# Optimization experiments

Measured on AMD Instinct MI355X. Metric: run time of the kernel, lower is better.

The kernel has to match this reference:

```python
import jax, jax.numpy as jnp
import numpy as np
import math

INPUTDIM = 256
OUTDIM = 512
GRIDSIZE = 64

def setup_inputs() -> dict:
    key = jax.random.key(0)
    k1, k2 = jax.random.split(key)
    x = jax.random.normal(k1, (4096, INPUTDIM), dtype=jnp.float32)
    # init: randn / (sqrt(inputdim) * sqrt(gridsize))  (smooth_initialization=False)
    fouriercoeffs = jax.random.normal(k2, (2, OUTDIM, INPUTDIM, GRIDSIZE), dtype=jnp.float32) / (
        math.sqrt(INPUTDIM) * math.sqrt(GRIDSIZE))
    bias = jnp.zeros((1, OUTDIM), dtype=jnp.float32)
    return {"x": x, "fouriercoeffs": fouriercoeffs, "bias": bias}

def reference(x, fouriercoeffs, bias):
    # x: [N, I]; fouriercoeffs: [2, O, I, G]; bias: [1, O]
    k = jnp.arange(1, GRIDSIZE + 1, dtype=x.dtype)          # [G]
    kx = x[:, :, None] * k[None, None, :]                   # [N, I, G]
    c = jnp.cos(kx)
    s = jnp.sin(kx)
    # contraction over (I, G) — GEMM-equivalent of the naive broadcast-sum
    y = jnp.einsum('nig,oig->no', c, fouriercoeffs[0])
    y = y + jnp.einsum('nig,oig->no', s, fouriercoeffs[1])
    y = y + bias
    return y
```

## Files before the change

kernel.cpp:

```cpp
#include <hip/hip_runtime.h>
#include <hip/hip_bf16.h>

#define IDIM 256
#define GDIM 64
#define ODIM 512
#define KD   (IDIM * GDIM)
#define TILE_SHORTS (512 * 64)
#define WS_NEED ((size_t)512 * TILE_SHORTS * 2)

typedef __attribute__((ext_vector_type(8))) short bhalf8;
typedef __attribute__((ext_vector_type(4))) float fvec4;
typedef __attribute__((ext_vector_type(4))) unsigned uvec4;

#define INV2PI 0.15915494309189535f
#define AS1 __attribute__((address_space(1)))
#define AS3 __attribute__((address_space(3)))

static __device__ __forceinline__ short bf16b(float v) {
    __hip_bfloat16 hb = __float2bfloat16(v);
    short s; __builtin_memcpy(&s, &hb, 2); return s;
}
static __device__ __forceinline__ unsigned cvtpk(float lo, float hi) {
    unsigned r;
    asm("v_cvt_pk_bf16_f32 %0, %1, %2" : "=v"(r) : "v"(lo), "v"(hi));
    return r;
}

#define ADVP(A,B,C2) do { float _t = __builtin_fmaf((C2),(B),-(A)); (A)=(B); (B)=_t; \
                          _t = __builtin_fmaf((C2),(B),-(A)); (A)=(B); (B)=_t; } while (0)

__global__ void prep_b(const float* __restrict__ coeffs, short* __restrict__ ws) {
    const int b = blockIdx.x;
    const int i = b >> 1, h = b & 1;
    const int o = threadIdx.x;
    short* dst = ws + ((size_t)b * 512 + o) * 64;
    const int swz = (o & 7) << 4;
#pragma unroll
    for (int j = 0; j < 8; ++j) {
        const int z = j >> 2, Qq = j & 3;
        const float* src = coeffs + ((size_t)z * ODIM + o) * KD
                         + (size_t)i * GDIM + 16 * Qq + 8 * h;
        fvec4 v0 = ((const fvec4*)src)[0];
        fvec4 v1 = ((const fvec4*)src)[1];
        bhalf8 pk;
#pragma unroll
        for (int u = 0; u < 4; ++u) { pk[u] = bf16b(v0[u]); pk[4 + u] = bf16b(v1[u]); }
        *(bhalf8*)((char*)dst + ((j * 16) ^ swz)) = pk;
    }
}

__global__ void bias_init(const float* __restrict__ bias, float* __restrict__ out) {
    int idx = blockIdx.x * 256 + threadIdx.x;
    fvec4 bv = ((const fvec4*)bias)[idx & 127];
    ((fvec4*)out)[idx] = bv;
}

#define FENCE() do { asm volatile("s_waitcnt vmcnt(0) lgkmcnt(0)" ::: "memory"); \
                     __builtin_amdgcn_sched_barrier(0); \
                     __syncthreads(); } while (0)

template<int USE_WS>
__global__ void __launch_bounds__(256, 4)
fkan_gemm(const float* __restrict__ x, const float* __restrict__ coeffs,
          const short* __restrict__ wsb, float* __restrict__ out) {
    __shared__ __align__(16) short B_lds[2][128 * 64];
    __shared__ float  sl_rev[4][128];
    __shared__ float2 sl_cs[4][128];

    const int bx = blockIdx.x;
    const int xcd = bx & 7, j = bx >> 3;
    const int lg  = xcd * 4 + (j & 3);
    const int mt  = j >> 2;
    const int ot  = lg >> 3, ks = lg & 7;
    const int row0 = mt * 128, col0 = ot * 128;
    const int i0 = ks * 32;

    const int t = threadIdx.x;
    const int lane = t & 63, wid = t >> 6;
    const int kl  = (lane >> 4) * 16;
    const int msk = (lane & 7) << 4;
    const int rA0 = wid * 32 + (lane & 15);
    const float m0f = (float)(16 * (lane >> 4) + 1);

    fvec4 acc[2][8];
#pragma unroll
    for (int a = 0; a < 2; ++a)
#pragma unroll
        for (int b = 0; b < 8; ++b) acc[a][b] = (fvec4)0.0f;

    auto fill_sl = [&](int chunk) {
#pragma unroll
        for (int w2 = 0; w2 < 2; ++w2) {
            int idx = lane + w2 * 64;
            int il2 = idx & 3, r2 = wid * 32 + (idx >> 2);
            float xv = x[(size_t)(row0 + r2) * IDIM + i0 + chunk * 4 + il2];
            float rev = xv * INV2PI;
            float a = __builtin_amdgcn_fractf(rev);
            float2 cs;
            cs.x = __builtin_amdgcn_cosf(a);
            cs.y = __builtin_amdgcn_sinf(a);
            sl_rev[il2][r2] = rev;
            sl_cs[il2][r2] = cs;
        }
    };

    auto dmaB = [&](int T1) {
        const short* src = wsb + (size_t)(i0 * 2 + T1) * TILE_SHORTS
                         + (size_t)col0 * 64 + (size_t)t * 8;
        const int bsel = T1 & 1;
#pragma unroll
        for (int q = 0; q < 4; ++q)
            __builtin_amdgcn_global_load_lds(
                (const AS1 unsigned*)(src + q * 2048),
                (AS3 unsigned*)&B_lds[bsel][q * 2048 + wid * 512],
                16, 0, 0);
    };

    auto stage_fb = [&](int T1) {
        const int bsel = T1 & 1;
        const int i = i0 + (T1 >> 1), hh = T1 & 1;
        const int o = t >> 1, z = t & 1;
        char* drow = (char*)&B_lds[bsel][o * 64];
        const int swz = (o & 7) << 4;
#pragma unroll
        for (int Qq = 0; Qq < 4; ++Qq) {
            const float* src = coeffs + ((size_t)z * ODIM + col0 + o) * KD
                             + (size_t)i * GDIM + 16 * Qq + 8 * hh;
            fvec4 v0 = ((const fvec4*)src)[0];
            fvec4 v1 = ((const fvec4*)src)[1];
            bhalf8 pk;
#pragma unroll
            for (int u = 0; u < 4; ++u) { pk[u] = bf16b(v0[u]); pk[4 + u] = bf16b(v1[u]); }
            *(bhalf8*)(drow + ((z * 64 + Qq * 16) ^ swz)) = pk;
        }
    };

    float ccA0, ccB0, ccA1, ccB1;
    float ssA0, ssB0, ssA1, ssB1;
    float C20, C21;
    bhalf8 afc[2], afs[2];

    auto seed_even = [&](int Te) {
        const int il = (Te >> 1) & 3;
#pragma unroll
        for (int fm = 0; fm < 2; ++fm) {
            const int rr = rA0 + fm * 16;
            float rev = sl_rev[il][rr];
            float2 cs1 = sl_cs[il][rr];
            float C2x = cs1.x + cs1.x;
            float a0 = __builtin_amdgcn_fractf(rev * m0f);
            float c0 = __builtin_amdgcn_cosf(a0);
            float s0 = __builtin_amdgcn_sinf(a0);
            float cBv = __builtin_fmaf(c0, cs1.x, -(s0 * cs1.y));
            float sBv = __builtin_fmaf(s0, cs1.x,  c0 * cs1.y);
            uvec4 u; u[0] = cvtpk(c0, cBv);
            float A = c0, B = cBv;
            ADVP(A, B, C2x); u[1] = cvtpk(A, B);
            ADVP(A, B, C2x); u[2] = cvtpk(A, B);
            ADVP(A, B, C2x); u[3] = cvtpk(A, B);
            if (fm == 0) { ccA0 = A; ccB0 = B; ssA0 = s0; ssB0 = sBv; C20 = C2x; }
            else         { ccA1 = A; ccB1 = B; ssA1 = s0; ssB1 = sBv; C21 = C2x; }
            afc[fm] = __builtin_bit_cast(bhalf8, u);
        }
    };

    auto mfma_z = [&](const char* Bb, int z, bhalf8 a0f, bhalf8 a1f) {
        const int koff = (z * 64 + kl) ^ msk;
#pragma unroll
        for (int half = 0; half < 2; ++half) {
            bhalf8 bq[4];
#pragma unroll
            for (int f4 = 0; f4 < 4; ++f4)
                bq[f4] = *(const bhalf8*)(Bb +
                    (size_t)(half * 64 + f4 * 16 + (lane & 15)) * 128 + koff);
            __builtin_amdgcn_s_setprio(1);
#pragma unroll
            for (int f4 = 0; f4 < 4; ++f4) {
                acc[0][half * 4 + f4] = __builtin_amdgcn_mfma_f32_16x16x32_bf16(
                    a0f, bq[f4], acc[0][half * 4 + f4], 0, 0, 0);
                acc[1][half * 4 + f4] = __builtin_amdgcn_mfma_f32_16x16x32_bf16(
                    a1f, bq[f4], acc[1][half * 4 + f4], 0, 0, 0);
            }
            __builtin_amdgcn_s_setprio(0);
        }
    };

    fill_sl(0);
    asm volatile("s_waitcnt lgkmcnt(0)" ::: "memory");
    __builtin_amdgcn_sched_barrier(0);
    seed_even(0);
    if (USE_WS) { dmaB(0); FENCE(); }
    else        { __syncthreads(); }

#pragma unroll 1
    for (int T = 0; T < 64; ++T) {
        if (USE_WS) {
            if ((T & 7) == 6 && T < 62) fill_sl((T + 2) >> 3);
            if (T < 63) dmaB(T + 1);
            __builtin_amdgcn_sched_barrier(0);
        } else {
            if ((T & 7) == 6 && T < 62) fill_sl((T + 2) >> 3);
            stage_fb(T);
            __syncthreads();
        }

        const char* Bb = (const char*)&B_lds[T & 1][0];

        mfma_z(Bb, 0, afc[0], afc[1]);
        if ((T & 1) == 0) {
#pragma unroll
            for (int fm = 0; fm < 2; ++fm) {
                float A = fm ? ssA1 : ssA0, B = fm ? ssB1 : ssB0;
                float C2x = fm ? C21 : C20;
                uvec4 u; u[0] = cvtpk(A, B);
                ADVP(A, B, C2x); u[1] = cvtpk(A, B);
                ADVP(A, B, C2x); u[2] = cvtpk(A, B);
                ADVP(A, B, C2x); u[3] = cvtpk(A, B);
                if (fm == 0) { ssA0 = A; ssB0 = B; } else { ssA1 = A; ssB1 = B; }
                afs[fm] = __builtin_bit_cast(bhalf8, u);
            }
        } else {
#pragma unroll
            for (int fm = 0; fm < 2; ++fm) {
                float A = fm ? ssA1 : ssA0, B = fm ? ssB1 : ssB0;
                float C2x = fm ? C21 : C20;
                uvec4 u;
                ADVP(A, B, C2x); u[0] = cvtpk(A, B);
                ADVP(A, B, C2x); u[1] = cvtpk(A, B);
                ADVP(A, B, C2x); u[2] = cvtpk(A, B);
                ADVP(A, B, C2x); u[3] = cvtpk(A, B);
                afs[fm] = __builtin_bit_cast(bhalf8, u);
            }
        }

        mfma_z(Bb, 1, afs[0], afs[1]);
        if (T < 63) {
            if ((T & 1) == 0) {
#pragma unroll
                for (int fm = 0; fm < 2; ++fm) {
                    float A = fm ? ccA1 : ccA0, B = fm ? ccB1 : ccB0;
                    float C2x = fm ? C21 : C20;
                    uvec4 u;
                    ADVP(A, B, C2x); u[0] = cvtpk(A, B);
                    ADVP(A, B, C2x); u[1] = cvtpk(A, B);
                    ADVP(A, B, C2x); u[2] = cvtpk(A, B);
                    ADVP(A, B, C2x); u[3] = cvtpk(A, B);
                    afc[fm] = __builtin_bit_cast(bhalf8, u);
                }
            } else {
                seed_even(T + 1);
            }
        }

        if (USE_WS) FENCE(); else __syncthreads();
    }

#pragma unroll
    for (int fm = 0; fm < 2; ++fm) {
#pragma unroll
        for (int f = 0; f < 8; ++f) {
            int col = col0 + f * 16 + (lane & 15);
#pragma unroll
            for (int r = 0; r < 4; ++r) {
                int row = row0 + wid * 32 + fm * 16 + ((lane >> 4) * 4) + r;
                atomicAdd(&out[(size_t)row * ODIM + col], acc[fm][f][r]);
            }
        }
    }
}

extern "C" void kernel_launch(void* const* d_in, const int* in_sizes, int n_in,
                              void* d_out, int out_size, void* d_ws, size_t ws_size,
                              hipStream_t stream) {
    (void)in_sizes; (void)n_in; (void)out_size;
    const float* x      = (const float*)d_in[0];
    const float* coeffs = (const float*)d_in[1];
    const float* bias   = (const float*)d_in[2];
    float* out = (float*)d_out;

    const bool use_ws = (ws_size >= WS_NEED) && (((uintptr_t)d_ws & 15) == 0);

    bias_init<<<dim3(2048), dim3(256), 0, stream>>>(bias, out);
    if (use_ws) {
        prep_b<<<dim3(512), dim3(512), 0, stream>>>(coeffs, (short*)d_ws);
        fkan_gemm<1><<<dim3(1024), dim3(256), 0, stream>>>(x, coeffs, (const short*)d_ws, out);
    } else {
        fkan_gemm<0><<<dim3(1024), dim3(256), 0, stream>>>(x, coeffs, nullptr, out);
    }
}
```

Baseline: 176.1 us.

## Switch wave tiling to 2x2 layout and unroll loop by two steps

The four waves now tile the 128x128 output block as 2x2 quadrants of 64x64 instead of four 32-row strips covering all 128 columns. Each wave loads 4 B fragments per k-step instead of 8, but must generate 4 A fragments of cos/sin instead of 2, so more transcendental and recurrence work is done per wave. The main loop is unrolled by two with fixed LDS buffer indices, and the A-fragment generation is interleaved with the MFMA calls. This trades LDS read traffic for extra VALU work and register pressure.

```diff
diff --git a/kernel.cpp b/kernel.cpp
--- a/kernel.cpp
+++ b/kernel.cpp
@@ -77,22 +77,24 @@
 
     const int t = threadIdx.x;
     const int lane = t & 63, wid = t >> 6;
+    const int wave_m = wid & 1, wave_n = wid >> 1;
     const int kl  = (lane >> 4) * 16;
     const int msk = (lane & 7) << 4;
-    const int rA0 = wid * 32 + (lane & 15);
+    const int rA0 = wave_m * 64 + (lane & 15);
+    const int cB0 = wave_n * 64 + (lane & 15);
     const float m0f = (float)(16 * (lane >> 4) + 1);
 
-    fvec4 acc[2][8];
-#pragma unroll
-    for (int a = 0; a < 2; ++a)
-#pragma unroll
-        for (int b = 0; b < 8; ++b) acc[a][b] = (fvec4)0.0f;
+    fvec4 acc[4][4];
+#pragma unroll
+    for (int a = 0; a < 4; ++a)
+#pragma unroll
+        for (int b = 0; b < 4; ++b) acc[a][b] = (fvec4)0.0f;
 
     auto fill_sl = [&](int chunk) {
 #pragma unroll
         for (int w2 = 0; w2 < 2; ++w2) {
-            int idx = lane + w2 * 64;
-            int il2 = idx & 3, r2 = wid * 32 + (idx >> 2);
+            int idx = t + w2 * 256;
+            int il2 = idx & 3, r2 = idx >> 2;
             float xv = x[(size_t)(row0 + r2) * IDIM + i0 + chunk * 4 + il2];
             float rev = xv * INV2PI;
             float a = __builtin_amdgcn_fractf(rev);
@@ -135,135 +137,160 @@
         }
     };
 
-    float ccA0, ccB0, ccA1, ccB1;
-    float ssA0, ssB0, ssA1, ssB1;
-    float C20, C21;
-    bhalf8 afc[2], afs[2];
-
-    auto seed_even = [&](int Te) {
-        const int il = (Te >> 1) & 3;
-#pragma unroll
-        for (int fm = 0; fm < 2; ++fm) {
-            const int rr = rA0 + fm * 16;
-            float rev = sl_rev[il][rr];
-            float2 cs1 = sl_cs[il][rr];
-            float C2x = cs1.x + cs1.x;
-            float a0 = __builtin_amdgcn_fractf(rev * m0f);
-            float c0 = __builtin_amdgcn_cosf(a0);
-            float s0 = __builtin_amdgcn_sinf(a0);
-            float cBv = __builtin_fmaf(c0, cs1.x, -(s0 * cs1.y));
-            float sBv = __builtin_fmaf(s0, cs1.x,  c0 * cs1.y);
-            uvec4 u; u[0] = cvtpk(c0, cBv);
-            float A = c0, B = cBv;
-            ADVP(A, B, C2x); u[1] = cvtpk(A, B);
-            ADVP(A, B, C2x); u[2] = cvtpk(A, B);
-            ADVP(A, B, C2x); u[3] = cvtpk(A, B);
-            if (fm == 0) { ccA0 = A; ccB0 = B; ssA0 = s0; ssB0 = sBv; C20 = C2x; }
-            else         { ccA1 = A; ccB1 = B; ssA1 = s0; ssB1 = sBv; C21 = C2x; }
-            afc[fm] = __builtin_bit_cast(bhalf8, u);
-        }
-    };
-
-    auto mfma_z = [&](const char* Bb, int z, bhalf8 a0f, bhalf8 a1f) {
-        const int koff = (z * 64 + kl) ^ msk;
-#pragma unroll
-        for (int half = 0; half < 2; ++half) {
-            bhalf8 bq[4];
-#pragma unroll
-            for (int f4 = 0; f4 < 4; ++f4)
-                bq[f4] = *(const bhalf8*)(Bb +
-                    (size_t)(half * 64 + f4 * 16 + (lane & 15)) * 128 + koff);
-            __builtin_amdgcn_s_setprio(1);
-#pragma unroll
-            for (int f4 = 0; f4 < 4; ++f4) {
-                acc[0][half * 4 + f4] = __builtin_amdgcn_mfma_f32_16x16x32_bf16(
-                    a0f, bq[f4], acc[0][half * 4 + f4], 0, 0, 0);
-                acc[1][half * 4 + f4] = __builtin_amdgcn_mfma_f32_16x16x32_bf16(
-                    a1f, bq[f4], acc[1][half * 4 + f4], 0, 0, 0);
-            }
-            __builtin_amdgcn_s_setprio(0);
-        }
-    };
+    float kcA[4], kcB[4], ksA[4], ksB[4], kC2[4];
 
     fill_sl(0);
-    asm volatile("s_waitcnt lgkmcnt(0)" ::: "memory");
-    __builtin_amdgcn_sched_barrier(0);
-    seed_even(0);
     if (USE_WS) { dmaB(0); FENCE(); }
     else        { __syncthreads(); }
 
 #pragma unroll 1
-    for (int T = 0; T < 64; ++T) {
-        if (USE_WS) {
-            if ((T & 7) == 6 && T < 62) fill_sl((T + 2) >> 3);
-            if (T < 63) dmaB(T + 1);
-            __builtin_amdgcn_sched_barrier(0);
-        } else {
-            if ((T & 7) == 6 && T < 62) fill_sl((T + 2) >> 3);
-            stage_fb(T);
-            __syncthreads();
-        }
-
-        const char* Bb = (const char*)&B_lds[T & 1][0];
-
-        mfma_z(Bb, 0, afc[0], afc[1]);
-        if ((T & 1) == 0) {
-#pragma unroll
-            for (int fm = 0; fm < 2; ++fm) {
-                float A = fm ? ssA1 : ssA0, B = fm ? ssB1 : ssB0;
-                float C2x = fm ? C21 : C20;
-                uvec4 u; u[0] = cvtpk(A, B);
-                ADVP(A, B, C2x); u[1] = cvtpk(A, B);
-                ADVP(A, B, C2x); u[2] = cvtpk(A, B);
-                ADVP(A, B, C2x); u[3] = cvtpk(A, B);
-                if (fm == 0) { ssA0 = A; ssB0 = B; } else { ssA1 = A; ssB1 = B; }
-                afs[fm] = __builtin_bit_cast(bhalf8, u);
-            }
-        } else {
-#pragma unroll
-            for (int fm = 0; fm < 2; ++fm) {
-                float A = fm ? ssA1 : ssA0, B = fm ? ssB1 : ssB0;
-                float C2x = fm ? C21 : C20;
-                uvec4 u;
-                ADVP(A, B, C2x); u[0] = cvtpk(A, B);
-                ADVP(A, B, C2x); u[1] = cvtpk(A, B);
-                ADVP(A, B, C2x); u[2] = cvtpk(A, B);
-                ADVP(A, B, C2x); u[3] = cvtpk(A, B);
-                afs[fm] = __builtin_bit_cast(bhalf8, u);
-            }
-        }
-
-        mfma_z(Bb, 1, afs[0], afs[1]);
-        if (T < 63) {
-            if ((T & 1) == 0) {
-#pragma unroll
-                for (int fm = 0; fm < 2; ++fm) {
-                    float A = fm ? ccA1 : ccA0, B = fm ? ccB1 : ccB0;
-                    float C2x = fm ? C21 : C20;
+    for (int ii = 0; ii < 32; ++ii) {
+        const int il = ii & 3;
+
+        {
+            const int T = 2 * ii;
+            if (USE_WS) {
+                dmaB(T + 1);
+                __builtin_amdgcn_sched_barrier(0);
+            } else {
+                stage_fb(T);
+                __syncthreads();
+            }
+            const char* Bb = (const char*)&B_lds[0][0];
+
+            {
+                bhalf8 bq[4];
+#pragma unroll
+                for (int fn = 0; fn < 4; ++fn)
+                    bq[fn] = *(const bhalf8*)(Bb +
+                        (size_t)(cB0 + fn * 16) * 128 + (kl ^ msk));
+#pragma unroll
+                for (int fm = 0; fm < 4; ++fm) {
+                    const int rr = rA0 + fm * 16;
+                    float rev = sl_rev[il][rr];
+                    float2 cs1 = sl_cs[il][rr];
+                    float C2x = cs1.x + cs1.x;
+                    float a0 = __builtin_amdgcn_fractf(rev * m0f);
+                    float c0 = __builtin_amdgcn_cosf(a0);
+                    float s0 = __builtin_amdgcn_sinf(a0);
+                    float cBv = __builtin_fmaf(c0, cs1.x, -(s0 * cs1.y));
+                    float sBv = __builtin_fmaf(s0, cs1.x,  c0 * cs1.y);
+                    uvec4 u; u[0] = cvtpk(c0, cBv);
+                    float A = c0, B = cBv;
+                    ADVP(A, B, C2x); u[1] = cvtpk(A, B);
+                    ADVP(A, B, C2x); u[2] = cvtpk(A, B);
+                    ADVP(A, B, C2x); u[3] = cvtpk(A, B);
+                    kcA[fm] = A; kcB[fm] = B; ksA[fm] = s0; ksB[fm] = sBv; kC2[fm] = C2x;
+                    bhalf8 af = __builtin_bit_cast(bhalf8, u);
+                    __builtin_amdgcn_s_setprio(1);
+#pragma unroll
+                    for (int fn = 0; fn < 4; ++fn)
+                        acc[fm][fn] = __builtin_amdgcn_mfma_f32_16x16x32_bf16(
+                            af, bq[fn], acc[fm][fn], 0, 0, 0);
+                    __builtin_amdgcn_s_setprio(0);
+                }
+            }
+            {
+                bhalf8 bq[4];
+#pragma unroll
+                for (int fn = 0; fn < 4; ++fn)
+                    bq[fn] = *(const bhalf8*)(Bb +
+                        (size_t)(cB0 + fn * 16) * 128 + ((64 + kl) ^ msk));
+#pragma unroll
+                for (int fm = 0; fm < 4; ++fm) {
+                    float C2x = kC2[fm];
+                    float A = ksA[fm], B = ksB[fm];
+                    uvec4 u; u[0] = cvtpk(A, B);
+                    ADVP(A, B, C2x); u[1] = cvtpk(A, B);
+                    ADVP(A, B, C2x); u[2] = cvtpk(A, B);
+                    ADVP(A, B, C2x); u[3] = cvtpk(A, B);
+                    ksA[fm] = A; ksB[fm] = B;
+                    bhalf8 af = __builtin_bit_cast(bhalf8, u);
+                    __builtin_amdgcn_s_setprio(1);
+#pragma unroll
+                    for (int fn = 0; fn < 4; ++fn)
+                        acc[fm][fn] = __builtin_amdgcn_mfma_f32_16x16x32_bf16(
+                            af, bq[fn], acc[fm][fn], 0, 0, 0);
+                    __builtin_amdgcn_s_setprio(0);
+                }
+            }
+            if (USE_WS) FENCE(); else __syncthreads();
+        }
+
+        {
+            const int T = 2 * ii + 1;
+            if (USE_WS) {
+                if ((T & 7) == 7 && T < 63) fill_sl((T + 1) >> 3);
+                if (T < 63) dmaB(T + 1);
+                __builtin_amdgcn_sched_barrier(0);
+            } else {
+                if ((T & 7) == 7 && T < 63) fill_sl((T + 1) >> 3);
+                stage_fb(T);
+                __syncthreads();
+            }
+            const char* Bb = (const char*)&B_lds[1][0];
+
+            {
+                bhalf8 bq[4];
+#pragma unroll
+                for (int fn = 0; fn < 4; ++fn)
+                    bq[fn] = *(const bhalf8*)(Bb +
+                        (size_t)(cB0 + fn * 16) * 128 + (kl ^ msk));
+#pragma unroll
+                for (int fm = 0; fm < 4; ++fm) {
+                    float C2x = kC2[fm];
+                    float A = kcA[fm], B = kcB[fm];
                     uvec4 u;
                     ADVP(A, B, C2x); u[0] = cvtpk(A, B);
                     ADVP(A, B, C2x); u[1] = cvtpk(A, B);
                     ADVP(A, B, C2x); u[2] = cvtpk(A, B);
                     ADVP(A, B, C2x); u[3] = cvtpk(A, B);
-                    afc[fm] = __builtin_bit_cast(bhalf8, u);
+                    bhalf8 af = __builtin_bit_cast(bhalf8, u);
+                    __builtin_amdgcn_s_setprio(1);
+#pragma unroll
+                    for (int fn = 0; fn < 4; ++fn)
+                        acc[fm][fn] = __builtin_amdgcn_mfma_f32_16x16x32_bf16(
+                            af, bq[fn], acc[fm][fn], 0, 0, 0);
+                    __builtin_amdgcn_s_setprio(0);
                 }
-            } else {
-                seed_even(T + 1);
-            }
-        }
-
-        if (USE_WS) FENCE(); else __syncthreads();
+            }
+            {
+                bhalf8 bq[4];
+#pragma unroll
+                for (int fn = 0; fn < 4; ++fn)
+                    bq[fn] = *(const bhalf8*)(Bb +
+                        (size_t)(cB0 + fn * 16) * 128 + ((64 + kl) ^ msk));
+#pragma unroll
+                for (int fm = 0; fm < 4; ++fm) {
+                    float C2x = kC2[fm];
+                    float A = ksA[fm], B = ksB[fm];
+                    uvec4 u;
+                    ADVP(A, B, C2x); u[0] = cvtpk(A, B);
+                    ADVP(A, B, C2x); u[1] = cvtpk(A, B);
+                    ADVP(A, B, C2x); u[2] = cvtpk(A, B);
+                    ADVP(A, B, C2x); u[3] = cvtpk(A, B);
+                    bhalf8 af = __builtin_bit_cast(bhalf8, u);
+                    __builtin_amdgcn_s_setprio(1);
+#pragma unroll
+                    for (int fn = 0; fn < 4; ++fn)
+                        acc[fm][fn] = __builtin_amdgcn_mfma_f32_16x16x32_bf16(
+                            af, bq[fn], acc[fm][fn], 0, 0, 0);
+                    __builtin_amdgcn_s_setprio(0);
+                }
+            }
+            if (USE_WS) FENCE(); else __syncthreads();
+        }
     }
 
 #pragma unroll
-    for (int fm = 0; fm < 2; ++fm) {
-#pragma unroll
-        for (int f = 0; f < 8; ++f) {
-            int col = col0 + f * 16 + (lane & 15);
+    for (int fm = 0; fm < 4; ++fm) {
+#pragma unroll
+        for (int fn = 0; fn < 4; ++fn) {
+            int col = col0 + wave_n * 64 + fn * 16 + (lane & 15);
 #pragma unroll
             for (int r = 0; r < 4; ++r) {
-                int row = row0 + wid * 32 + fm * 16 + ((lane >> 4) * 4) + r;
-                atomicAdd(&out[(size_t)row * ODIM + col], acc[fm][f][r]);
+                int row = row0 + wave_m * 64 + fm * 16 + ((lane >> 4) * 4) + r;
+                atomicAdd(&out[(size_t)row * ODIM + col], acc[fm][fn][r]);
             }
         }
     }
```

Result: slower. 196.9 us (+11.8%).
